# Kernel tuning notes

Measured on AMD Instinct MI355X. Metric: run time of the kernel, lower is better.

The kernel has to match this reference:

```python
import jax, jax.numpy as jnp
import numpy as np

D_MODEL = 1024
DK = 64
N_HEADS = D_MODEL // DK
MASK = True


def setup_inputs() -> dict:
    key = jax.random.key(0)
    ks = jax.random.split(key, 8)
    B, S = 4, 2048
    scale = 1.0 / np.sqrt(D_MODEL)
    return {
        "query_data": jax.random.normal(ks[0], (B, S, D_MODEL), dtype=jnp.float32),
        "key_data": jax.random.normal(ks[1], (B, S, D_MODEL), dtype=jnp.float32),
        "value_data": jax.random.normal(ks[2], (B, S, D_MODEL), dtype=jnp.float32),
        "Wq": jax.random.normal(ks[3], (D_MODEL, D_MODEL), dtype=jnp.float32) * scale,
        "Wk": jax.random.normal(ks[4], (D_MODEL, D_MODEL), dtype=jnp.float32) * scale,
        "Wv": jax.random.normal(ks[5], (D_MODEL, D_MODEL), dtype=jnp.float32) * scale,
        "Wp": jax.random.normal(ks[6], (D_MODEL, D_MODEL), dtype=jnp.float32) * scale,
        "bp": jnp.zeros((D_MODEL,), dtype=jnp.float32),
    }


def reference(query_data, key_data, value_data, Wq, Wk, Wv, Wp, bp):
    B, S, _ = query_data.shape
    # QKV projections, split into heads: (B, H, S, dk)
    def split_heads(x, W):
        return (x @ W.T).reshape(B, -1, N_HEADS, DK).transpose(0, 2, 1, 3)

    q = split_heads(query_data, Wq)
    k = split_heads(key_data, Wk)
    v = split_heads(value_data, Wv)

    scores = jnp.einsum("bhqd,bhkd->bhqk", q, k) / np.sqrt(DK).astype(np.float32)
    if MASK:
        Sq, Sk = scores.shape[-2], scores.shape[-1]
        causal = jnp.triu(jnp.ones((Sq, Sk), dtype=scores.dtype), k=1) * jnp.float32(-1e13)
        scores = scores + causal  # broadcast over (B, H)
    attn = jax.nn.softmax(scores, axis=-1)
    out = jnp.einsum("bhqk,bhkd->bhqd", attn, v)
    out = out.transpose(0, 2, 1, 3).reshape(B, S, D_MODEL)
    # dropout is identity in eval mode
    return out @ Wp.T + bp
```

## Files before the change

kernel.cpp:

```cpp
#include <hip/hip_runtime.h>
#include <hip/hip_bf16.h>
#include <stdint.h>

#define D_MODEL 1024
#define SEQ     2048
#define BATCH   4
#define NH      16
#define DKK     64
#define MROWS   (BATCH * SEQ)

typedef unsigned short u16;
using bf16x8 = __attribute__((ext_vector_type(8))) __bf16;
using f32x4  = __attribute__((ext_vector_type(4))) float;

__device__ __forceinline__ u16 f2bf(float f) {
    union { float f; uint32_t u; } v; v.f = f;
    return (u16)((v.u + 0x7FFFu + ((v.u >> 16) & 1u)) >> 16);
}
__device__ __forceinline__ uint32_t pk2bf(float a, float b) {
    union { __hip_bfloat162 h; uint32_t u; } v;
    v.h = __float22bfloat162_rn(float2{a, b});
    return v.u;
}

__device__ __forceinline__ float fast_exp2(float x) {
    float r; asm("v_exp_f32 %0, %1" : "=v"(r) : "v"(x)); return r;
}
__device__ __forceinline__ float fast_rcp(float x) {
    float r; asm("v_rcp_f32 %0, %1" : "=v"(r) : "v"(x)); return r;
}

__device__ __forceinline__ void gl_lds16(const u16* g, u16* l) {
    __builtin_amdgcn_global_load_lds(
        (__attribute__((address_space(1))) void*)(const_cast<u16*>(g)),
        (__attribute__((address_space(3))) void*)l, 16, 0, 0);
}

__device__ __forceinline__ int stage_col8(int lane) {
    return (((lane & 3) ^ ((lane >> 3) & 3)) * 8);
}
__device__ __forceinline__ int frag_off(int row, int quad, int l15) {
    return row * 32 + ((quad ^ ((l15 >> 1) & 3)) * 8);
}

__device__ __forceinline__ int swz(int o, int n) {
    const int pos = ((n >> 3) ^ (o & 15)) ^ (((o >> 4) & 1) << 2);
    return o * 128 + (pos << 3) + (n & 7);
}
__device__ __forceinline__ int swzg(int o, int gn) {
    const int pos = (gn ^ (o & 15)) ^ (((o >> 4) & 1) << 2);
    return o * 128 + (pos << 3);
}

__global__ __launch_bounds__(256) void cvt_all(const float* __restrict__ a,
                                               const float* __restrict__ b,
                                               const float* __restrict__ c,
                                               const float* __restrict__ wq,
                                               const float* __restrict__ wk,
                                               const float* __restrict__ wv,
                                               const float* __restrict__ wp,
                                               u16* __restrict__ da, u16* __restrict__ db,
                                               u16* __restrict__ dc, u16* __restrict__ dq,
                                               u16* __restrict__ dk, u16* __restrict__ dv,
                                               u16* __restrict__ dp) {
    const int i = blockIdx.x * 256 + threadIdx.x;
    const float* s; u16* d; int off;
    if (i < 3 * (1 << 21)) {
        const int sel = i >> 21; off = i & ((1 << 21) - 1);
        s = (sel == 0) ? a : (sel == 1) ? b : c;
        d = (sel == 0) ? da : (sel == 1) ? db : dc;
    } else {
        const int j = i - 3 * (1 << 21);
        const int sel = j >> 18; off = j & ((1 << 18) - 1);
        s = (sel == 0) ? wq : (sel == 1) ? wk : (sel == 2) ? wv : wp;
        d = (sel == 0) ? dq : (sel == 1) ? dk : (sel == 2) ? dv : dp;
    }
    float4 v = ((const float4*)s)[off];
    uint2 o;
    o.x = pk2bf(v.x, v.y); o.y = pk2bf(v.z, v.w);
    ((uint2*)d)[off] = o;
}

__global__ __launch_bounds__(256, 3) void gemm_qkv(const u16* __restrict__ XQ,
                                                   const u16* __restrict__ XK,
                                                   const u16* __restrict__ XV,
                                                   const u16* __restrict__ WQ,
                                                   const u16* __restrict__ WK,
                                                   const u16* __restrict__ WV,
                                                   u16* __restrict__ Qo,
                                                   u16* __restrict__ Ko,
                                                   u16* __restrict__ Vto) {
    constexpr int K = 1024, N = 1024;
    __shared__ __align__(16) u16 smem[16384];
    u16* ldsA = smem;
    u16* ldsB = smem + 8192;
    u16* ldsT = smem;

    const int which = blockIdx.x >> 9;
    const int inner = blockIdx.x & 511;
    const u16* A  = (which == 0) ? XQ : (which == 1) ? XK : XV;
    const u16* Bw = (which == 0) ? WQ : (which == 1) ? WK : WV;

    const int t = threadIdx.x;
    const int w = t >> 6, lane = t & 63;
    const int quad = lane >> 4, l15 = lane & 15;
    const int x = inner & 7, j = inner >> 3;
    const int bm = x * 8 + (j >> 3), bn = j & 7;
    const int wm = (w >> 1) * 64, wn = (w & 1) * 64;

    const u16* Ab = A  + (size_t)bm * 128 * K;
    const u16* Bb = Bw + (size_t)bn * 128 * K;
    const int srow  = lane >> 2;
    const int sc8   = stage_col8(lane);

    f32x4 acc[4][4];
    #pragma unroll
    for (int i = 0; i < 4; ++i)
        #pragma unroll
        for (int jj = 0; jj < 4; ++jj)
            acc[i][jj] = f32x4{0.f, 0.f, 0.f, 0.f};

    #pragma unroll
    for (int i = 0; i < 2; ++i) {
        const int c = w * 2 + i;
        gl_lds16(Ab + (size_t)(c * 16 + srow) * K + sc8, &ldsA[c * 512]);
        gl_lds16(Bb + (size_t)(c * 16 + srow) * K + sc8, &ldsB[c * 512]);
    }

    int cur = 0;
    for (int k0 = 0; k0 < K; k0 += 32) {
        __syncthreads();
        if (k0 + 32 < K) {
            const int nxt = cur ^ 1;
            #pragma unroll
            for (int i = 0; i < 2; ++i) {
                const int c = w * 2 + i;
                gl_lds16(Ab + (size_t)(c * 16 + srow) * K + k0 + 32 + sc8, &ldsA[nxt * 4096 + c * 512]);
                gl_lds16(Bb + (size_t)(c * 16 + srow) * K + k0 + 32 + sc8, &ldsB[nxt * 4096 + c * 512]);
            }
        }

        bf16x8 afr[4], bfr[4];
        #pragma unroll
        for (int i = 0; i < 4; ++i)
            afr[i] = *(const bf16x8*)&ldsA[cur * 4096 + frag_off(wm + i * 16 + l15, quad, l15)];
        #pragma unroll
        for (int jj = 0; jj < 4; ++jj)
            bfr[jj] = *(const bf16x8*)&ldsB[cur * 4096 + frag_off(wn + jj * 16 + l15, quad, l15)];

        #pragma unroll
        for (int i = 0; i < 4; ++i)
            #pragma unroll
            for (int jj = 0; jj < 4; ++jj)
                acc[i][jj] = __builtin_amdgcn_mfma_f32_16x16x32_bf16(afr[i], bfr[jj], acc[i][jj], 0, 0, 0);
        cur ^= 1;
    }

    __syncthreads();

    if (which < 2) {
        u16* outb = which ? Ko : Qo;
        #pragma unroll
        for (int i = 0; i < 4; ++i)
            #pragma unroll
            for (int jj = 0; jj < 4; ++jj)
                #pragma unroll
                for (int r = 0; r < 4; ++r)
                    ldsT[swz(wm + i * 16 + quad * 4 + r, wn + jj * 16 + l15)] = f2bf(acc[i][jj][r]);
        __syncthreads();
        const int rr = t >> 1, half = t & 1;
        u16* dstg = outb + (size_t)(bm * 128 + rr) * N + bn * 128;
        #pragma unroll
        for (int k = 0; k < 8; ++k) {
            const int gn = half * 8 + k;
            *(uint4*)(dstg + gn * 8) = *(const uint4*)&ldsT[swzg(rr, gn)];
        }
    } else {
        #pragma unroll
        for (int i = 0; i < 4; ++i)
            #pragma unroll
            for (int jj = 0; jj < 4; ++jj)
                #pragma unroll
                for (int r = 0; r < 4; ++r)
                    ldsT[swz(wn + jj * 16 + l15, wm + i * 16 + quad * 4 + r)] = f2bf(acc[i][jj][r]);
        __syncthreads();
        const int c = t >> 1, half = t & 1;
        const int colg = bn * 128 + c;
        const int hh = colg >> 6, dd = colg & 63;
        const int bb = bm >> 4;
        const int s0 = (bm * 128) & 2047;
        u16* dstg = Vto + (size_t)((bb * NH + hh) * DKK + dd) * SEQ + s0;
        #pragma unroll
        for (int k = 0; k < 8; ++k) {
            const int gn = half * 8 + k;
            *(uint4*)(dstg + gn * 8) = *(const uint4*)&ldsT[swzg(c, gn)];
        }
    }
}

__global__ __launch_bounds__(256, 4) void gemm_proj(const u16* __restrict__ A,
                                                    const u16* __restrict__ Bw,
                                                    float* __restrict__ outf,
                                                    const float* __restrict__ bias) {
    constexpr int K = 1024, N = 1024;
    __shared__ __align__(16) u16 ldsA[2 * 2048];
    __shared__ __align__(16) u16 ldsB[2 * 4096];

    const int t = threadIdx.x;
    const int w = t >> 6, lane = t & 63;
    const int quad = lane >> 4, l15 = lane & 15;
    const int x = blockIdx.x & 7, j = blockIdx.x >> 3;
    const int bm = x * 16 + (j >> 3), bn = j & 7;
    const int wm = (w >> 1) * 32, wn = (w & 1) * 64;

    const u16* Ab = A  + (size_t)bm * 64 * K;
    const u16* Bb = Bw + (size_t)bn * 128 * K;
    const int srow  = lane >> 2;
    const int sc8   = stage_col8(lane);

    f32x4 acc[2][4];
    #pragma unroll
    for (int i = 0; i < 2; ++i)
        #pragma unroll
        for (int jj = 0; jj < 4; ++jj)
            acc[i][jj] = f32x4{0.f, 0.f, 0.f, 0.f};

    gl_lds16(Ab + (size_t)(w * 16 + srow) * K + sc8, &ldsA[w * 512]);
    #pragma unroll
    for (int i = 0; i < 2; ++i) {
        const int c = w * 2 + i;
        gl_lds16(Bb + (size_t)(c * 16 + srow) * K + sc8, &ldsB[c * 512]);
    }

    int cur = 0;
    for (int k0 = 0; k0 < K; k0 += 32) {
        __syncthreads();
        if (k0 + 32 < K) {
            const int nxt = cur ^ 1;
            gl_lds16(Ab + (size_t)(w * 16 + srow) * K + k0 + 32 + sc8, &ldsA[nxt * 2048 + w * 512]);
            #pragma unroll
            for (int i = 0; i < 2; ++i) {
                const int c = w * 2 + i;
                gl_lds16(Bb + (size_t)(c * 16 + srow) * K + k0 + 32 + sc8, &ldsB[nxt * 4096 + c * 512]);
            }
        }

        bf16x8 afr[2], bfr[4];
        #pragma unroll
        for (int i = 0; i < 2; ++i)
            afr[i] = *(const bf16x8*)&ldsA[cur * 2048 + frag_off(wm + i * 16 + l15, quad, l15)];
        #pragma unroll
        for (int jj = 0; jj < 4; ++jj)
            bfr[jj] = *(const bf16x8*)&ldsB[cur * 4096 + frag_off(wn + jj * 16 + l15, quad, l15)];

        #pragma unroll
        for (int i = 0; i < 2; ++i)
            #pragma unroll
            for (int jj = 0; jj < 4; ++jj)
                acc[i][jj] = __builtin_amdgcn_mfma_f32_16x16x32_bf16(afr[i], bfr[jj], acc[i][jj], 0, 0, 0);
        cur ^= 1;
    }

    #pragma unroll
    for (int i = 0; i < 2; ++i)
        #pragma unroll
        for (int jj = 0; jj < 4; ++jj)
            #pragma unroll
            for (int r = 0; r < 4; ++r) {
                const int row = bm * 64 + wm + i * 16 + quad * 4 + r;
                const int col = bn * 128 + wn + jj * 16 + l15;
                outf[(size_t)row * N + col] = acc[i][jj][r] + bias[col];
            }
}

__global__ __launch_bounds__(256, 3) void flash_attn(const u16* __restrict__ Qb,
                                                     const u16* __restrict__ Kb,
                                                     const u16* __restrict__ Vt,
                                                     u16* __restrict__ O) {
    __shared__ __align__(16) u16 ldsK[2 * 4096];
    __shared__ __align__(16) u16 ldsV[2 * 4096];
    __shared__ __align__(16) u16 ldsP[4 * 2048];

    const int t = threadIdx.x;
    const int w = t >> 6, lane = t & 63;
    const int quad = lane >> 4, l15 = lane & 15;
    const int bh = blockIdx.x & 63;
    const int qt = 15 - (blockIdx.x >> 6);
    const int b = bh >> 4, h = bh & 15;
    const int q0 = qt * 128;
    const int qw = q0 + w * 32;

    const int srow  = lane >> 2;
    const int sc8   = stage_col8(lane);
    const size_t kbase = (size_t)b * SEQ * D_MODEL + h * DKK;
    const size_t vbase = (size_t)(bh * DKK) * SEQ;

    bf16x8 qf[2][2];
    #pragma unroll
    for (int g = 0; g < 2; ++g) {
        const u16* Qrow = Qb + (size_t)(b * SEQ + qw + g * 16 + l15) * D_MODEL + h * DKK;
        qf[g][0] = *(const bf16x8*)(Qrow + quad * 8);
        qf[g][1] = *(const bf16x8*)(Qrow + 32 + quad * 8);
    }

    f32x4 o_acc[2][4];
    #pragma unroll
    for (int g = 0; g < 2; ++g)
        #pragma unroll
        for (int nt = 0; nt < 4; ++nt) o_acc[g][nt] = f32x4{0.f, 0.f, 0.f, 0.f};
    float l_i[2] = {0.f, 0.f};

    const float C2 = 0.18033688f;
    u16* PwS = &ldsP[w * 2048];

    const int ntiles = 2 * qt + 2;

    #pragma unroll
    for (int i = 0; i < 2; ++i) {
        const int e = w * 2 + i, ch = e >> 2, rb = (e & 3) * 16;
        gl_lds16(Kb + kbase + (size_t)(rb + srow) * D_MODEL + ch * 32 + sc8,
                 &ldsK[ch * 2048 + rb * 32]);
        gl_lds16(Vt + vbase + (size_t)(rb + srow) * SEQ + ch * 32 + sc8,
                 &ldsV[ch * 2048 + rb * 32]);
    }

    int cur = 0;
    for (int it = 0; it < ntiles; ++it) {
        const int kb = it * 64;
        __syncthreads();

        if (it + 1 < ntiles) {
            const int nb = kb + 64, nxt = cur ^ 1;
            #pragma unroll
            for (int i = 0; i < 2; ++i) {
                const int e = w * 2 + i, ch = e >> 2, rb = (e & 3) * 16;
                gl_lds16(Kb + kbase + (size_t)(nb + rb + srow) * D_MODEL + ch * 32 + sc8,
                         &ldsK[nxt * 4096 + ch * 2048 + rb * 32]);
                gl_lds16(Vt + vbase + (size_t)(rb + srow) * SEQ + nb + ch * 32 + sc8,
                         &ldsV[nxt * 4096 + ch * 2048 + rb * 32]);
            }
        }

        if (kb <= qw + 31) {
            f32x4 sc[2][4];
            #pragma unroll
            for (int g = 0; g < 2; ++g)
                #pragma unroll
                for (int jt = 0; jt < 4; ++jt) sc[g][jt] = f32x4{0.f, 0.f, 0.f, 0.f};
            #pragma unroll
            for (int ks = 0; ks < 2; ++ks)
                #pragma unroll
                for (int jt = 0; jt < 4; ++jt) {
                    bf16x8 kf = *(const bf16x8*)&ldsK[cur * 4096 + ks * 2048 + frag_off(jt * 16 + l15, quad, l15)];
                    #pragma unroll
                    for (int g = 0; g < 2; ++g)
                        sc[g][jt] = __builtin_amdgcn_mfma_f32_16x16x32_bf16(kf, qf[g][ks], sc[g][jt], 0, 0, 0);
                }

            if (kb + 63 >= qw) {
                #pragma unroll
                for (int g = 0; g < 2; ++g)
                    #pragma unroll
                    for (int jt = 0; jt < 4; ++jt)
                        #pragma unroll
                        for (int r = 0; r < 4; ++r)
                            if (kb + jt * 16 + quad * 4 + r > qw + g * 16 + l15) sc[g][jt][r] = -3.0e38f;
            }

            #pragma unroll
            for (int g = 0; g < 2; ++g) {
                float tsum = 0.f;
                #pragma unroll
                for (int jt = 0; jt < 4; ++jt) {
                    float p[4];
                    #pragma unroll
                    for (int r = 0; r < 4; ++r) {
                        p[r] = fast_exp2(sc[g][jt][r] * C2);
                        tsum += p[r];
                    }
                    const int pos = (4 * jt + quad) ^ l15;
                    uint2 pk;
                    pk.x = pk2bf(p[0], p[1]);
                    pk.y = pk2bf(p[2], p[3]);
                    *(uint2*)&PwS[g * 1024 + l15 * 64 + pos * 4] = pk;
                }
                tsum += __shfl_xor(tsum, 16);
                tsum += __shfl_xor(tsum, 32);
                l_i[g] += tsum;
            }

            asm volatile("s_waitcnt lgkmcnt(0)" ::: "memory");

            #pragma unroll
            for (int ks = 0; ks < 2; ++ks) {
                const int gg = 8 * ks + 2 * quad;
                union { bf16x8 v; uint2 u[2]; } pu[2];
                #pragma unroll
                for (int g = 0; g < 2; ++g) {
                    pu[g].u[0] = *(const uint2*)&PwS[g * 1024 + l15 * 64 + ((gg) ^ l15) * 4];
                    pu[g].u[1] = *(const uint2*)&PwS[g * 1024 + l15 * 64 + ((gg + 1) ^ l15) * 4];
                }
                #pragma unroll
                for (int nt = 0; nt < 4; ++nt) {
                    bf16x8 vf = *(const bf16x8*)&ldsV[cur * 4096 + ks * 2048 + frag_off(nt * 16 + l15, quad, l15)];
                    #pragma unroll
                    for (int g = 0; g < 2; ++g)
                        o_acc[g][nt] = __builtin_amdgcn_mfma_f32_16x16x32_bf16(pu[g].v, vf, o_acc[g][nt], 0, 0, 0);
                }
            }
        }

        cur ^= 1;
    }

    __syncthreads();
    u16* ldsO = ldsK;
    #pragma unroll
    for (int g = 0; g < 2; ++g) {
        const float rli = fast_rcp(l_i[g]);
        float rl[4];
        #pragma unroll
        for (int r = 0; r < 4; ++r)
            rl[r] = __shfl(rli, (lane & 48) | (quad * 4 + r));
        #pragma unroll
        for (int nt = 0; nt < 4; ++nt)
            #pragma unroll
            for (int r = 0; r < 4; ++r) {
                const int row = w * 32 + g * 16 + quad * 4 + r;
                ldsO[row * 64 + nt * 16 + l15] = f2bf(o_acc[g][nt][r] * rl[r]);
            }
    }
    __syncthreads();
    #pragma unroll
    for (int it2 = 0; it2 < 4; ++it2) {
        const int row = it2 * 32 + (t >> 3);
        const uint4 v = *(const uint4*)&ldsO[row * 64 + (t & 7) * 8];
        *(uint4*)(O + (size_t)(b * SEQ + q0 + row) * D_MODEL + h * DKK + (t & 7) * 8) = v;
    }
}

extern "C" void kernel_launch(void* const* d_in, const int* in_sizes, int n_in,
                              void* d_out, int out_size, void* d_ws, size_t ws_size,
                              hipStream_t stream) {
    const float* q_in = (const float*)d_in[0];
    const float* k_in = (const float*)d_in[1];
    const float* v_in = (const float*)d_in[2];
    const float* Wq   = (const float*)d_in[3];
    const float* Wk   = (const float*)d_in[4];
    const float* Wv   = (const float*)d_in[5];
    const float* Wp   = (const float*)d_in[6];
    const float* bp   = (const float*)d_in[7];
    float* out = (float*)d_out;

    char* ws = (char*)d_ws;
    u16* XQ  = (u16*)(ws + (size_t)0);
    u16* XK  = (u16*)(ws + ((size_t)16 << 20));
    u16* XV  = (u16*)(ws + ((size_t)32 << 20));
    u16* WQb = (u16*)(ws + ((size_t)48 << 20));
    u16* WKb = (u16*)(ws + ((size_t)50 << 20));
    u16* WVb = (u16*)(ws + ((size_t)52 << 20));
    u16* WPb = (u16*)(ws + ((size_t)54 << 20));
    u16* Qb  = (u16*)(ws + ((size_t)56 << 20));
    u16* Kb  = (u16*)(ws + ((size_t)72 << 20));
    u16* Vtb = (u16*)(ws + ((size_t)88 << 20));

    const int n4 = 3 * (1 << 21) + 4 * (1 << 18);
    cvt_all<<<n4 / 256, 256, 0, stream>>>(q_in, k_in, v_in, Wq, Wk, Wv, Wp,
                                          XQ, XK, XV, WQb, WKb, WVb, WPb);

    gemm_qkv<<<1536, 256, 0, stream>>>(XQ, XK, XV, WQb, WKb, WVb, Qb, Kb, Vtb);

    flash_attn<<<BATCH * NH * (SEQ / 128), 256, 0, stream>>>(Qb, Kb, Vtb, XQ);

    gemm_proj<<<1024, 256, 0, stream>>>(XQ, WPb, out, bp);
}
```

Measured before the change: 310.1 us.

## Split attention KV tiles across waves with LDS reduction; enlarge projection GEMM tile

The flash attention kernel now gives each block a 64-row query tile. Its four waves each take a strided subset of the KV tiles, each with private K/V LDS buffers and a synchronous load-then-wait per tile, and the per-wave partial outputs and row sums are reduced through LDS at the end. This replaces the shared double-buffered pipeline and the per-wave causal skip, and aims to balance causal work and double the block count. The output projection GEMM moves from a 64x128 to a 128x128 tile per block with a 4x4 accumulator per wave, which gives more reuse per LDS load at the cost of lower occupancy. Risks are that the KV loads are no longer overlapped with compute, and that the fp32 reduction needs more LDS.

```diff
diff --git a/kernel.cpp b/kernel.cpp
--- a/kernel.cpp
+++ b/kernel.cpp
@@ -41,6 +41,10 @@
 }
 __device__ __forceinline__ int frag_off(int row, int quad, int l15) {
     return row * 32 + ((quad ^ ((l15 >> 1) & 3)) * 8);
+}
+
+__device__ __forceinline__ int fstage_g8(int lane) {
+    return (((lane & 7) ^ ((lane >> 3) & 7)) * 8);
 }
 
 __device__ __forceinline__ int swz(int o, int n) {
@@ -198,37 +202,38 @@
     }
 }
 
-__global__ __launch_bounds__(256, 4) void gemm_proj(const u16* __restrict__ A,
+__global__ __launch_bounds__(256, 3) void gemm_proj(const u16* __restrict__ A,
                                                     const u16* __restrict__ Bw,
                                                     float* __restrict__ outf,
                                                     const float* __restrict__ bias) {
     constexpr int K = 1024, N = 1024;
-    __shared__ __align__(16) u16 ldsA[2 * 2048];
-    __shared__ __align__(16) u16 ldsB[2 * 4096];
+    __shared__ __align__(16) u16 smem[16384];
+    u16* ldsA = smem;
+    u16* ldsB = smem + 8192;
 
     const int t = threadIdx.x;
     const int w = t >> 6, lane = t & 63;
     const int quad = lane >> 4, l15 = lane & 15;
     const int x = blockIdx.x & 7, j = blockIdx.x >> 3;
-    const int bm = x * 16 + (j >> 3), bn = j & 7;
-    const int wm = (w >> 1) * 32, wn = (w & 1) * 64;
-
-    const u16* Ab = A  + (size_t)bm * 64 * K;
+    const int bm = x * 8 + (j >> 3), bn = j & 7;
+    const int wm = (w >> 1) * 64, wn = (w & 1) * 64;
+
+    const u16* Ab = A  + (size_t)bm * 128 * K;
     const u16* Bb = Bw + (size_t)bn * 128 * K;
     const int srow  = lane >> 2;
     const int sc8   = stage_col8(lane);
 
-    f32x4 acc[2][4];
-    #pragma unroll
-    for (int i = 0; i < 2; ++i)
+    f32x4 acc[4][4];
+    #pragma unroll
+    for (int i = 0; i < 4; ++i)
         #pragma unroll
         for (int jj = 0; jj < 4; ++jj)
             acc[i][jj] = f32x4{0.f, 0.f, 0.f, 0.f};
 
-    gl_lds16(Ab + (size_t)(w * 16 + srow) * K + sc8, &ldsA[w * 512]);
     #pragma unroll
     for (int i = 0; i < 2; ++i) {
         const int c = w * 2 + i;
+        gl_lds16(Ab + (size_t)(c * 16 + srow) * K + sc8, &ldsA[c * 512]);
         gl_lds16(Bb + (size_t)(c * 16 + srow) * K + sc8, &ldsB[c * 512]);
     }
 
@@ -237,24 +242,24 @@
         __syncthreads();
         if (k0 + 32 < K) {
             const int nxt = cur ^ 1;
-            gl_lds16(Ab + (size_t)(w * 16 + srow) * K + k0 + 32 + sc8, &ldsA[nxt * 2048 + w * 512]);
             #pragma unroll
             for (int i = 0; i < 2; ++i) {
                 const int c = w * 2 + i;
+                gl_lds16(Ab + (size_t)(c * 16 + srow) * K + k0 + 32 + sc8, &ldsA[nxt * 4096 + c * 512]);
                 gl_lds16(Bb + (size_t)(c * 16 + srow) * K + k0 + 32 + sc8, &ldsB[nxt * 4096 + c * 512]);
             }
         }
 
-        bf16x8 afr[2], bfr[4];
-        #pragma unroll
-        for (int i = 0; i < 2; ++i)
-            afr[i] = *(const bf16x8*)&ldsA[cur * 2048 + frag_off(wm + i * 16 + l15, quad, l15)];
+        bf16x8 afr[4], bfr[4];
+        #pragma unroll
+        for (int i = 0; i < 4; ++i)
+            afr[i] = *(const bf16x8*)&ldsA[cur * 4096 + frag_off(wm + i * 16 + l15, quad, l15)];
         #pragma unroll
         for (int jj = 0; jj < 4; ++jj)
             bfr[jj] = *(const bf16x8*)&ldsB[cur * 4096 + frag_off(wn + jj * 16 + l15, quad, l15)];
 
         #pragma unroll
-        for (int i = 0; i < 2; ++i)
+        for (int i = 0; i < 4; ++i)
             #pragma unroll
             for (int jj = 0; jj < 4; ++jj)
                 acc[i][jj] = __builtin_amdgcn_mfma_f32_16x16x32_bf16(afr[i], bfr[jj], acc[i][jj], 0, 0, 0);
@@ -262,113 +267,100 @@
     }
 
     #pragma unroll
-    for (int i = 0; i < 2; ++i)
+    for (int i = 0; i < 4; ++i)
         #pragma unroll
         for (int jj = 0; jj < 4; ++jj)
             #pragma unroll
             for (int r = 0; r < 4; ++r) {
-                const int row = bm * 64 + wm + i * 16 + quad * 4 + r;
+                const int row = bm * 128 + wm + i * 16 + quad * 4 + r;
                 const int col = bn * 128 + wn + jj * 16 + l15;
                 outf[(size_t)row * N + col] = acc[i][jj][r] + bias[col];
             }
 }
 
-__global__ __launch_bounds__(256, 3) void flash_attn(const u16* __restrict__ Qb,
+__global__ __launch_bounds__(256, 2) void flash_attn(const u16* __restrict__ Qb,
                                                      const u16* __restrict__ Kb,
                                                      const u16* __restrict__ Vt,
                                                      u16* __restrict__ O) {
-    __shared__ __align__(16) u16 ldsK[2 * 4096];
-    __shared__ __align__(16) u16 ldsV[2 * 4096];
+    __shared__ __align__(16) u16 ldsKV[8 * 4096];
     __shared__ __align__(16) u16 ldsP[4 * 2048];
 
     const int t = threadIdx.x;
     const int w = t >> 6, lane = t & 63;
     const int quad = lane >> 4, l15 = lane & 15;
     const int bh = blockIdx.x & 63;
-    const int qt = 15 - (blockIdx.x >> 6);
+    const int qt = 31 - (blockIdx.x >> 6);
     const int b = bh >> 4, h = bh & 15;
-    const int q0 = qt * 128;
-    const int qw = q0 + w * 32;
-
-    const int srow  = lane >> 2;
-    const int sc8   = stage_col8(lane);
+    const int q0 = qt * 64;
+    const int ntiles = qt + 1;
+
+    const int g8 = fstage_g8(lane);
+    const int r8 = lane >> 3;
     const size_t kbase = (size_t)b * SEQ * D_MODEL + h * DKK;
     const size_t vbase = (size_t)(bh * DKK) * SEQ;
 
-    bf16x8 qf[2][2];
-    #pragma unroll
-    for (int g = 0; g < 2; ++g) {
-        const u16* Qrow = Qb + (size_t)(b * SEQ + qw + g * 16 + l15) * D_MODEL + h * DKK;
+    u16* myK = &ldsKV[w * 4096];
+    u16* myV = &ldsKV[(4 + w) * 4096];
+    u16* PwS = &ldsP[w * 2048];
+
+    bf16x8 qf[4][2];
+    #pragma unroll
+    for (int g = 0; g < 4; ++g) {
+        const u16* Qrow = Qb + (size_t)(b * SEQ + q0 + g * 16 + l15) * D_MODEL + h * DKK;
         qf[g][0] = *(const bf16x8*)(Qrow + quad * 8);
         qf[g][1] = *(const bf16x8*)(Qrow + 32 + quad * 8);
     }
 
-    f32x4 o_acc[2][4];
-    #pragma unroll
-    for (int g = 0; g < 2; ++g)
+    f32x4 o_acc[4][4];
+    #pragma unroll
+    for (int g = 0; g < 4; ++g)
         #pragma unroll
         for (int nt = 0; nt < 4; ++nt) o_acc[g][nt] = f32x4{0.f, 0.f, 0.f, 0.f};
-    float l_i[2] = {0.f, 0.f};
+    float l_i[4] = {0.f, 0.f, 0.f, 0.f};
 
     const float C2 = 0.18033688f;
-    u16* PwS = &ldsP[w * 2048];
-
-    const int ntiles = 2 * qt + 2;
-
-    #pragma unroll
-    for (int i = 0; i < 2; ++i) {
-        const int e = w * 2 + i, ch = e >> 2, rb = (e & 3) * 16;
-        gl_lds16(Kb + kbase + (size_t)(rb + srow) * D_MODEL + ch * 32 + sc8,
-                 &ldsK[ch * 2048 + rb * 32]);
-        gl_lds16(Vt + vbase + (size_t)(rb + srow) * SEQ + ch * 32 + sc8,
-                 &ldsV[ch * 2048 + rb * 32]);
-    }
-
-    int cur = 0;
-    for (int it = 0; it < ntiles; ++it) {
-        const int kb = it * 64;
-        __syncthreads();
-
-        if (it + 1 < ntiles) {
-            const int nb = kb + 64, nxt = cur ^ 1;
-            #pragma unroll
-            for (int i = 0; i < 2; ++i) {
-                const int e = w * 2 + i, ch = e >> 2, rb = (e & 3) * 16;
-                gl_lds16(Kb + kbase + (size_t)(nb + rb + srow) * D_MODEL + ch * 32 + sc8,
-                         &ldsK[nxt * 4096 + ch * 2048 + rb * 32]);
-                gl_lds16(Vt + vbase + (size_t)(rb + srow) * SEQ + nb + ch * 32 + sc8,
-                         &ldsV[nxt * 4096 + ch * 2048 + rb * 32]);
-            }
-        }
-
-        if (kb <= qw + 31) {
-            f32x4 sc[2][4];
-            #pragma unroll
-            for (int g = 0; g < 2; ++g)
-                #pragma unroll
-                for (int jt = 0; jt < 4; ++jt) sc[g][jt] = f32x4{0.f, 0.f, 0.f, 0.f};
-            #pragma unroll
-            for (int ks = 0; ks < 2; ++ks)
-                #pragma unroll
-                for (int jt = 0; jt < 4; ++jt) {
-                    bf16x8 kf = *(const bf16x8*)&ldsK[cur * 4096 + ks * 2048 + frag_off(jt * 16 + l15, quad, l15)];
+
+    for (int tile = w; tile < ntiles; tile += 4) {
+        const int s0 = tile * 64;
+
+        #pragma unroll
+        for (int i = 0; i < 8; ++i)
+            gl_lds16(Kb + kbase + (size_t)(s0 + i * 8 + r8) * D_MODEL + g8, &myK[i * 512]);
+        #pragma unroll
+        for (int i = 0; i < 8; ++i)
+            gl_lds16(Vt + vbase + (size_t)(i * 8 + r8) * SEQ + s0 + g8, &myV[i * 512]);
+        asm volatile("s_waitcnt vmcnt(0)" ::: "memory");
+
+        f32x4 sc[4][4];
+        #pragma unroll
+        for (int g = 0; g < 4; ++g)
+            #pragma unroll
+            for (int jt = 0; jt < 4; ++jt) sc[g][jt] = f32x4{0.f, 0.f, 0.f, 0.f};
+        #pragma unroll
+        for (int ks = 0; ks < 2; ++ks)
+            #pragma unroll
+            for (int jt = 0; jt < 4; ++jt) {
+                bf16x8 kf = *(const bf16x8*)&myK[(jt * 16 + l15) * 64 + (((ks * 4 + quad) ^ (l15 & 7)) << 3)];
+                #pragma unroll
+                for (int g = 0; g < 4; ++g)
+                    sc[g][jt] = __builtin_amdgcn_mfma_f32_16x16x32_bf16(kf, qf[g][ks], sc[g][jt], 0, 0, 0);
+            }
+
+        if (tile == ntiles - 1) {
+            #pragma unroll
+            for (int g = 0; g < 4; ++g)
+                #pragma unroll
+                for (int jt = 0; jt < 4; ++jt)
                     #pragma unroll
-                    for (int g = 0; g < 2; ++g)
-                        sc[g][jt] = __builtin_amdgcn_mfma_f32_16x16x32_bf16(kf, qf[g][ks], sc[g][jt], 0, 0, 0);
-                }
-
-            if (kb + 63 >= qw) {
-                #pragma unroll
-                for (int g = 0; g < 2; ++g)
-                    #pragma unroll
-                    for (int jt = 0; jt < 4; ++jt)
-                        #pragma unroll
-                        for (int r = 0; r < 4; ++r)
-                            if (kb + jt * 16 + quad * 4 + r > qw + g * 16 + l15) sc[g][jt][r] = -3.0e38f;
-            }
-
-            #pragma unroll
-            for (int g = 0; g < 2; ++g) {
+                    for (int r = 0; r < 4; ++r)
+                        if (jt * 16 + quad * 4 + r > g * 16 + l15) sc[g][jt][r] = -3.0e38f;
+        }
+
+        #pragma unroll
+        for (int gp = 0; gp < 2; ++gp) {
+            #pragma unroll
+            for (int gl = 0; gl < 2; ++gl) {
+                const int g = gp * 2 + gl;
                 float tsum = 0.f;
                 #pragma unroll
                 for (int jt = 0; jt < 4; ++jt) {
@@ -382,7 +374,7 @@
                     uint2 pk;
                     pk.x = pk2bf(p[0], p[1]);
                     pk.y = pk2bf(p[2], p[3]);
-                    *(uint2*)&PwS[g * 1024 + l15 * 64 + pos * 4] = pk;
+                    *(uint2*)&PwS[gl * 1024 + l15 * 64 + pos * 4] = pk;
                 }
                 tsum += __shfl_xor(tsum, 16);
                 tsum += __shfl_xor(tsum, 32);
@@ -396,47 +388,59 @@
                 const int gg = 8 * ks + 2 * quad;
                 union { bf16x8 v; uint2 u[2]; } pu[2];
                 #pragma unroll
-                for (int g = 0; g < 2; ++g) {
-                    pu[g].u[0] = *(const uint2*)&PwS[g * 1024 + l15 * 64 + ((gg) ^ l15) * 4];
-                    pu[g].u[1] = *(const uint2*)&PwS[g * 1024 + l15 * 64 + ((gg + 1) ^ l15) * 4];
+                for (int gl = 0; gl < 2; ++gl) {
+                    pu[gl].u[0] = *(const uint2*)&PwS[gl * 1024 + l15 * 64 + ((gg) ^ l15) * 4];
+                    pu[gl].u[1] = *(const uint2*)&PwS[gl * 1024 + l15 * 64 + ((gg + 1) ^ l15) * 4];
                 }
                 #pragma unroll
                 for (int nt = 0; nt < 4; ++nt) {
-                    bf16x8 vf = *(const bf16x8*)&ldsV[cur * 4096 + ks * 2048 + frag_off(nt * 16 + l15, quad, l15)];
+                    bf16x8 vf = *(const bf16x8*)&myV[(nt * 16 + l15) * 64 + (((ks * 4 + quad) ^ (l15 & 7)) << 3)];
                     #pragma unroll
-                    for (int g = 0; g < 2; ++g)
-                        o_acc[g][nt] = __builtin_amdgcn_mfma_f32_16x16x32_bf16(pu[g].v, vf, o_acc[g][nt], 0, 0, 0);
+                    for (int gl = 0; gl < 2; ++gl)
+                        o_acc[gp * 2 + gl][nt] = __builtin_amdgcn_mfma_f32_16x16x32_bf16(pu[gl].v, vf, o_acc[gp * 2 + gl][nt], 0, 0, 0);
                 }
             }
         }
-
-        cur ^= 1;
     }
 
     __syncthreads();
-    u16* ldsO = ldsK;
-    #pragma unroll
-    for (int g = 0; g < 2; ++g) {
-        const float rli = fast_rcp(l_i[g]);
-        float rl[4];
-        #pragma unroll
-        for (int r = 0; r < 4; ++r)
-            rl[r] = __shfl(rli, (lane & 48) | (quad * 4 + r));
+    float* ldsO = (float*)ldsKV;
+    float* ldsL = (float*)ldsP;
+    #pragma unroll
+    for (int g = 0; g < 4; ++g) {
         #pragma unroll
         for (int nt = 0; nt < 4; ++nt)
             #pragma unroll
             for (int r = 0; r < 4; ++r) {
-                const int row = w * 32 + g * 16 + quad * 4 + r;
-                ldsO[row * 64 + nt * 16 + l15] = f2bf(o_acc[g][nt][r] * rl[r]);
-            }
+                const int q = g * 16 + quad * 4 + r;
+                ldsO[w * 4096 + q * 64 + nt * 16 + l15] = o_acc[g][nt][r];
+            }
+        if (quad == 0) ldsL[w * 1024 + g * 16 + l15] = l_i[g];
     }
     __syncthreads();
-    #pragma unroll
-    for (int it2 = 0; it2 < 4; ++it2) {
-        const int row = it2 * 32 + (t >> 3);
-        const uint4 v = *(const uint4*)&ldsO[row * 64 + (t & 7) * 8];
-        *(uint4*)(O + (size_t)(b * SEQ + q0 + row) * D_MODEL + h * DKK + (t & 7) * 8) = v;
-    }
+
+    const int q = t >> 2, dseg = (t & 3) * 16;
+    float accv[16];
+    #pragma unroll
+    for (int e = 0; e < 16; ++e) accv[e] = 0.f;
+    #pragma unroll
+    for (int w4 = 0; w4 < 4; ++w4) {
+        #pragma unroll
+        for (int ee = 0; ee < 4; ++ee) {
+            const f32x4 v = *(const f32x4*)&ldsO[w4 * 4096 + q * 64 + dseg + ee * 4];
+            accv[ee * 4 + 0] += v[0]; accv[ee * 4 + 1] += v[1];
+            accv[ee * 4 + 2] += v[2]; accv[ee * 4 + 3] += v[3];
+        }
+    }
+    const float ltot = ldsL[q] + ldsL[1024 + q] + ldsL[2048 + q] + ldsL[3072 + q];
+    const float rli = fast_rcp(ltot);
+    uint32_t pk[8];
+    #pragma unroll
+    for (int e = 0; e < 8; ++e)
+        pk[e] = pk2bf(accv[e * 2] * rli, accv[e * 2 + 1] * rli);
+    u16* dst = O + (size_t)(b * SEQ + q0 + q) * D_MODEL + h * DKK + dseg;
+    *(uint4*)dst       = *(const uint4*)&pk[0];
+    *(uint4*)(dst + 8) = *(const uint4*)&pk[4];
 }
 
 extern "C" void kernel_launch(void* const* d_in, const int* in_sizes, int n_in,
@@ -470,7 +474,7 @@
 
     gemm_qkv<<<1536, 256, 0, stream>>>(XQ, XK, XV, WQb, WKb, WVb, Qb, Kb, Vtb);
 
-    flash_attn<<<BATCH * NH * (SEQ / 128), 256, 0, stream>>>(Qb, Kb, Vtb, XQ);
-
-    gemm_proj<<<1024, 256, 0, stream>>>(XQ, WPb, out, bp);
-}
+    flash_attn<<<64 * (SEQ / 64), 256, 0, stream>>>(Qb, Kb, Vtb, XQ);
+
+    gemm_proj<<<512, 256, 0, stream>>>(XQ, WPb, out, bp);
+}
```

Result: no change. 315.4 us (+1.7%).
